# Performance work log

Hardware: AMD Instinct MI355X
Metric: run time of the kernel (lower is better)

Reference implementation:

```python
import jax, jax.numpy as jnp
import numpy as np
from jax import lax

B_, C_, H_, W_ = 2, 128, 64, 64
N_LAYERS = 2
D_STATE = 16
D_INNER = 2 * C_          # mamba expand=2
D_CONV = 4
DT_RANK = (C_ + 15) // 16  # ceil(d_model/16) = 8


def _layernorm(x, g, b, eps=1e-5):
    m = jnp.mean(x, axis=-1, keepdims=True)
    v = jnp.mean(jnp.square(x - m), axis=-1, keepdims=True)
    return (x - m) * lax.rsqrt(v + eps) * g + b


def _mamba(x, in_w, conv_w, conv_b, xproj_w, dt_w, dt_b, A_log, ssm_D, out_w):
    # x: (B, L, C)
    B, L, C = x.shape
    di, N = A_log.shape
    R = dt_w.shape[1]
    xz = x @ in_w.T                              # (B, L, 2*di)
    u, z = jnp.split(xz, 2, axis=-1)
    # causal depthwise conv1d, kernel d_conv, left-pad d_conv-1
    uc = u.transpose(0, 2, 1)                    # (B, di, L)
    uc = lax.conv_general_dilated(uc, conv_w, (1,), [(D_CONV - 1, 0)],
                                  feature_group_count=di)
    uc = uc + conv_b[None, :, None]
    u = jax.nn.silu(uc.transpose(0, 2, 1))       # (B, L, di)
    dbl = u @ xproj_w.T                          # (B, L, R+2N)
    dt, Bm, Cm = jnp.split(dbl, [R, R + N], axis=-1)
    dt = jax.nn.softplus(dt @ dt_w.T + dt_b)     # (B, L, di)
    A = -jnp.exp(A_log)                          # (di, N)
    dA = jnp.exp(dt[..., None] * A)              # (B, L, di, N)
    dBu = (dt * u)[..., None] * Bm[:, :, None, :]  # (B, L, di, N)

    def step(h, inp):
        dA_t, dBu_t, C_t = inp
        h = dA_t * h + dBu_t                     # (B, di, N)
        y = jnp.einsum('bdn,bn->bd', h, C_t)
        return h, y

    h0 = jnp.zeros((B, di, N), x.dtype)
    _, ys = lax.scan(step, h0, (dA.transpose(1, 0, 2, 3),
                                dBu.transpose(1, 0, 2, 3),
                                Cm.transpose(1, 0, 2)))
    y = ys.transpose(1, 0, 2) + u * ssm_D        # (B, L, di)
    y = y * jax.nn.silu(z)
    return y @ out_w.T                           # (B, L, C)


def setup_inputs() -> dict:
    key = jax.random.key(0)
    ks = jax.random.split(key, 24)
    C, di, N, R, L4 = C_, D_INNER, D_STATE, DT_RANK, 4 * C_
    s = lambda f: 1.0 / np.sqrt(f)
    inp = {
        'x': jax.random.normal(ks[0], (B_, C_, H_, W_), jnp.float32),
        'embed_w': jax.random.normal(ks[1], (C, C), jnp.float32) * s(C),
        'embed_b': jnp.zeros((C,), jnp.float32),
        'outc_w': jax.random.normal(ks[2], (C, C), jnp.float32) * s(C),
        'outc_b': jnp.zeros((C,), jnp.float32),
        'ln_g': jnp.ones((N_LAYERS, C), jnp.float32),
        'ln_b': jnp.zeros((N_LAYERS, C), jnp.float32),
        'in_w': jax.random.normal(ks[3], (N_LAYERS, 2 * di, C), jnp.float32) * s(C),
        'conv_w': jax.random.normal(ks[4], (N_LAYERS, di, 1, D_CONV), jnp.float32) * s(D_CONV),
        'conv_b': jnp.zeros((N_LAYERS, di), jnp.float32),
        'xproj_w': jax.random.normal(ks[5], (N_LAYERS, R + 2 * N, di), jnp.float32) * s(di),
        'dtproj_w': jax.random.normal(ks[6], (N_LAYERS, di, R), jnp.float32) * s(R),
        'dtproj_b': jax.random.uniform(ks[7], (N_LAYERS, di), jnp.float32, -4.0, -2.0),
        'A_log': jnp.tile(jnp.log(jnp.arange(1, N + 1, dtype=jnp.float32))[None, None, :],
                          (N_LAYERS, di, 1)),
        'ssm_D': jnp.ones((N_LAYERS, di), jnp.float32),
        'mout_w': jax.random.normal(ks[8], (N_LAYERS, C, di), jnp.float32) * s(di),
        'ffn_w1': jax.random.normal(ks[9], (N_LAYERS, L4, C), jnp.float32) * s(C),
        'ffn_b1': jnp.zeros((N_LAYERS, L4), jnp.float32),
        'ffn_w2': jax.random.normal(ks[10], (N_LAYERS, C, L4), jnp.float32) * s(L4),
        'ffn_b2': jnp.zeros((N_LAYERS, C), jnp.float32),
    }
    return inp


def reference(x, embed_w, embed_b, outc_w, outc_b, ln_g, ln_b, in_w, conv_w,
              conv_b, xproj_w, dtproj_w, dtproj_b, A_log, ssm_D, mout_w,
              ffn_w1, ffn_b1, ffn_w2, ffn_b2):
    B, C, H, W = x.shape
    residual = x
    h = jnp.einsum('bchw,oc->bohw', x, embed_w) + embed_b[None, :, None, None]
    t = h.reshape(B, C, H * W).transpose(0, 2, 1)   # (B, L, C)
    for i in range(N_LAYERS):
        r = t
        t2 = _layernorm(t, ln_g[i], ln_b[i])
        t2 = _mamba(t2, in_w[i], conv_w[i], conv_b[i], xproj_w[i],
                    dtproj_w[i], dtproj_b[i], A_log[i], ssm_D[i], mout_w[i])
        t = t2 + r
        r = t
        t2 = _layernorm(t, ln_g[i], ln_b[i])  # same LN params reused (as in source)
        t2 = jax.nn.gelu(t2 @ ffn_w1[i].T + ffn_b1[i], approximate=False)
        t2 = t2 @ ffn_w2[i].T + ffn_b2[i]
        t = t2 + r
    y = t.transpose(0, 2, 1).reshape(B, C, H, W)
    y = jnp.einsum('bchw,oc->bohw', y, outc_w) + outc_b[None, :, None, None]
    return residual + y
```

## Files before the change

kernel.cpp:

```cpp
#include <hip/hip_runtime.h>
#include <hip/hip_bf16.h>


#define LSEQ 4096
#define BLC  8192
#define NC   64
#define CHK  64
#define NCH  8192

typedef __attribute__((ext_vector_type(4))) float f32x4;
typedef __attribute__((ext_vector_type(8))) short s16x8;

__device__ __forceinline__ unsigned short f2bu(float f) {
    unsigned u = __float_as_uint(f);
    return (unsigned short)((u + 0x7fffu + ((u >> 16) & 1u)) >> 16);
}

template<bool ADD>
__global__ __launch_bounds__(256) void transpose_kernel(
    const float* __restrict__ in_, float* __restrict__ out_,
    const float* __restrict__ add, int R, int Cc)
{
    __shared__ float tile[32][33];
    size_t boff = (size_t)blockIdx.z * R * Cc;
    int r0 = blockIdx.y * 32, c0 = blockIdx.x * 32;
    int tx = threadIdx.x, ty = threadIdx.y;
#pragma unroll
    for (int j = 0; j < 4; ++j)
        tile[ty + j * 8][tx] = in_[boff + (size_t)(r0 + ty + j * 8) * Cc + (c0 + tx)];
    __syncthreads();
#pragma unroll
    for (int j = 0; j < 4; ++j) {
        size_t idx = boff + (size_t)(c0 + ty + j * 8) * R + (r0 + tx);
        float v = tile[tx][ty + j * 8];
        if (ADD) v += add[idx];
        out_[idx] = v;
    }
}

__global__ __launch_bounds__(256) void transposeDT(
    const float* __restrict__ dt, const float* __restrict__ u,
    float* __restrict__ dtT, float* __restrict__ dtuT)
{
    __shared__ float t1[32][33];
    __shared__ float t2[32][33];
    int r0 = blockIdx.y * 32, c0 = blockIdx.x * 32;
    int tx = threadIdx.x, ty = threadIdx.y;
#pragma unroll
    for (int j = 0; j < 4; ++j) {
        size_t idx = (size_t)(r0 + ty + j * 8) * 256 + (c0 + tx);
        float a = dt[idx], b = u[idx];
        t1[ty + j * 8][tx] = a;
        t2[ty + j * 8][tx] = a * b;
    }
    __syncthreads();
#pragma unroll
    for (int j = 0; j < 4; ++j) {
        size_t o = (size_t)(c0 + ty + j * 8) * BLC + (r0 + tx);
        dtT [o] = t1[tx][ty + j * 8];
        dtuT[o] = t2[tx][ty + j * 8];
    }
}

template<int BM, int ACT, bool BIAS, bool RES, bool SPLIT, bool EPI>
__global__ __launch_bounds__(256) void mgemm(
    const float* __restrict__ X, const float* __restrict__ W,
    const float* __restrict__ bias, const float* __restrict__ res,
    const float* __restrict__ pu, const float* __restrict__ pz,
    const float* __restrict__ pD,
    float* __restrict__ Y, float* __restrict__ Y2, int N, int K)
{
    constexpr int MF = BM / 32;
    __shared__ __align__(16) unsigned short Xs[BM * 64];
    __shared__ __align__(16) unsigned short Ws[64 * 64];
    int tid  = threadIdx.x;
    int lane = tid & 63;
    int wave = tid >> 6;
    int wm = wave >> 1, wn = wave & 1;
    int l15 = lane & 15, l4 = lane >> 4;
    int bm = blockIdx.x * BM, bn = blockIdx.y * 64;
    f32x4 acc[MF][2] = {};

    int q  = tid & 15;
    int r0 = tid >> 4;

    for (int k0 = 0; k0 < K; k0 += 64) {
        __syncthreads();
#pragma unroll
        for (int p = 0; p < BM / 16; ++p) {
            int row = r0 + p * 16;
            size_t gi = (size_t)(bm + row) * K + k0 + q * 4;
            float4 v = *(const float4*)&X[gi];
            if (EPI) {
                float4 u4 = *(const float4*)&pu[gi];
                float4 z4 = *(const float4*)&pz[gi];
                float4 D4 = *(const float4*)&pD[k0 + q * 4];
                v.x = fmaf(u4.x, D4.x, v.x) * (z4.x / (1.f + __expf(-z4.x)));
                v.y = fmaf(u4.y, D4.y, v.y) * (z4.y / (1.f + __expf(-z4.y)));
                v.z = fmaf(u4.z, D4.z, v.z) * (z4.z / (1.f + __expf(-z4.z)));
                v.w = fmaf(u4.w, D4.w, v.w) * (z4.w / (1.f + __expf(-z4.w)));
            }
            unsigned lo = f2bu(v.x) | ((unsigned)f2bu(v.y) << 16);
            unsigned hi = f2bu(v.z) | ((unsigned)f2bu(v.w) << 16);
            int off = (row * 128 + q * 8) ^ ((row & 7) << 4);
            *(uint2*)((char*)Xs + off) = make_uint2(lo, hi);
        }
#pragma unroll
        for (int p = 0; p < 4; ++p) {
            int row = r0 + p * 16;
            float4 v = *(const float4*)&W[(size_t)(bn + row) * K + k0 + q * 4];
            unsigned lo = f2bu(v.x) | ((unsigned)f2bu(v.y) << 16);
            unsigned hi = f2bu(v.z) | ((unsigned)f2bu(v.w) << 16);
            int off = (row * 128 + q * 8) ^ ((row & 7) << 4);
            *(uint2*)((char*)Ws + off) = make_uint2(lo, hi);
        }
        __syncthreads();
#pragma unroll
        for (int ks = 0; ks < 2; ++ks) {
            s16x8 a[MF], b[2];
#pragma unroll
            for (int mf = 0; mf < MF; ++mf) {
                int row = wm * (BM / 2) + mf * 16 + l15;
                int off = (row * 128 + (ks * 32 + l4 * 8) * 2) ^ ((row & 7) << 4);
                a[mf] = *(const s16x8*)((const char*)Xs + off);
            }
#pragma unroll
            for (int nf = 0; nf < 2; ++nf) {
                int row = wn * 32 + nf * 16 + l15;
                int off = (row * 128 + (ks * 32 + l4 * 8) * 2) ^ ((row & 7) << 4);
                b[nf] = *(const s16x8*)((const char*)Ws + off);
            }
#pragma unroll
            for (int mf = 0; mf < MF; ++mf)
#pragma unroll
                for (int nf = 0; nf < 2; ++nf)
                    acc[mf][nf] = __builtin_amdgcn_mfma_f32_16x16x32_bf16(
                        a[mf], b[nf], acc[mf][nf], 0, 0, 0);
        }
    }

#pragma unroll
    for (int mf = 0; mf < MF; ++mf) {
#pragma unroll
        for (int nf = 0; nf < 2; ++nf) {
            int col   = bn + wn * 32 + nf * 16 + l15;
            int rbase = bm + wm * (BM / 2) + mf * 16 + l4 * 4;
            float bv = BIAS ? bias[col] : 0.f;
#pragma unroll
            for (int r = 0; r < 4; ++r) {
                float v = acc[mf][nf][r] + bv;
                if (ACT == 2) v = 0.5f * v * (1.f + erff(v * 0.70710678118654752f));
                if (SPLIT) {
                    if (col < 256) Y [(size_t)(rbase + r) * 256 + col]       = v;
                    else           Y2[(size_t)(rbase + r) * 256 + col - 256] = v;
                } else {
                    size_t o = (size_t)(rbase + r) * N + col;
                    if (RES) v += res[o];
                    Y[o] = v;
                }
            }
        }
    }
}

template<int ACT, bool BIAS>
__global__ __launch_bounds__(256) void gemm_kernel(
    const float* __restrict__ X, int lda,
    const float* __restrict__ W,
    const float* __restrict__ bias,
    float* __restrict__ Y, int N, int K)
{
    __shared__ __align__(16) float As[16][68];
    __shared__ __align__(16) float Ws[16][68];
    int bm = blockIdx.x * 64;
    int bn = blockIdx.y * 64;
    int tid = threadIdx.x;
    int tm = (tid >> 4) << 2;
    int tn = (tid & 15) << 2;
    float acc[4][4] = {};

    for (int k0 = 0; k0 < K; k0 += 16) {
#pragma unroll
        for (int i = 0; i < 4; ++i) {
            int idx = tid + i * 256;
            int m  = idx >> 4;
            int kk = idx & 15;
            int gk = k0 + kk;
            As[kk][m] = (gk < K) ? X[(size_t)(bm + m) * lda + gk] : 0.f;
            int gn = bn + m;
            Ws[kk][m] = (gk < K && gn < N) ? W[(size_t)gn * K + gk] : 0.f;
        }
        __syncthreads();
#pragma unroll
        for (int kk = 0; kk < 16; ++kk) {
            float4 av = *reinterpret_cast<const float4*>(&As[kk][tm]);
            float4 bv = *reinterpret_cast<const float4*>(&Ws[kk][tn]);
            float a[4] = {av.x, av.y, av.z, av.w};
            float b[4] = {bv.x, bv.y, bv.z, bv.w};
#pragma unroll
            for (int i2 = 0; i2 < 4; ++i2)
#pragma unroll
                for (int j2 = 0; j2 < 4; ++j2)
                    acc[i2][j2] = fmaf(a[i2], b[j2], acc[i2][j2]);
        }
        __syncthreads();
    }
#pragma unroll
    for (int i2 = 0; i2 < 4; ++i2) {
        int gm = bm + tm + i2;
#pragma unroll
        for (int j2 = 0; j2 < 4; ++j2) {
            int gn = bn + tn + j2;
            if (gn < N) {
                float v = acc[i2][j2];
                if (BIAS) v += bias[gn];
                if (ACT == 1) v = (v > 0.f) ? v + log1pf(expf(-v)) : log1pf(expf(v));
                Y[(size_t)gm * N + gn] = v;
            }
        }
    }
}

__global__ __launch_bounds__(256) void ln_kernel(
    const float* __restrict__ X, const float* __restrict__ g,
    const float* __restrict__ bb, float* __restrict__ Y)
{
    int row  = blockIdx.x * 4 + (threadIdx.x >> 6);
    int lane = threadIdx.x & 63;
    const float* xr = X + (size_t)row * 128;
    float v0 = xr[lane], v1 = xr[lane + 64];
    float s = v0 + v1;
#pragma unroll
    for (int off = 32; off > 0; off >>= 1) s += __shfl_xor(s, off, 64);
    float mean = s * 0.0078125f;
    float d0 = v0 - mean, d1 = v1 - mean;
    float q = d0 * d0 + d1 * d1;
#pragma unroll
    for (int off = 32; off > 0; off >>= 1) q += __shfl_xor(q, off, 64);
    float rstd = rsqrtf(q * 0.0078125f + 1e-5f);
    float* yr = Y + (size_t)row * 128;
    yr[lane]      = d0 * rstd * g[lane]      + bb[lane];
    yr[lane + 64] = d1 * rstd * g[lane + 64] + bb[lane + 64];
}

__global__ __launch_bounds__(256) void conv_silu_kernel(
    const float* __restrict__ u, const float* __restrict__ cw,
    const float* __restrict__ cb, float* __restrict__ out)
{
    int i   = blockIdx.x * 256 + threadIdx.x;
    int dq  = (i & 63) << 2;
    int row = i >> 6;
    int l   = row & (LSEQ - 1);
    float4 a = *(const float4*)&cb[dq];
    float w[4][4];
#pragma unroll
    for (int e = 0; e < 4; ++e) {
        float4 we = *(const float4*)&cw[(dq + e) * 4];
        w[e][0] = we.x; w[e][1] = we.y; w[e][2] = we.z; w[e][3] = we.w;
    }
#pragma unroll
    for (int j = 0; j < 4; ++j) {
        if (l >= 3 - j) {
            const float4 v = *(const float4*)&u[(size_t)(row - 3 + j) * 256 + dq];
            a.x = fmaf(v.x, w[0][j], a.x);
            a.y = fmaf(v.y, w[1][j], a.y);
            a.z = fmaf(v.z, w[2][j], a.z);
            a.w = fmaf(v.w, w[3][j], a.w);
        }
    }
    float4 o;
    o.x = a.x / (1.f + __expf(-a.x));
    o.y = a.y / (1.f + __expf(-a.y));
    o.z = a.z / (1.f + __expf(-a.z));
    o.w = a.w / (1.f + __expf(-a.w));
    *(float4*)&out[(size_t)row * 256 + dq] = o;
}

__global__ __launch_bounds__(256) void scan_phase1(
    const float* __restrict__ dtT, const float* __restrict__ dtuT,
    const float* __restrict__ dbl, const float* __restrict__ A_log,
    float* __restrict__ hend, float* __restrict__ aprod)
{
    int g    = threadIdx.x & 3;
    int dloc = threadIdx.x >> 2;
    int d    = blockIdx.x * 64 + dloc;
    int c    = blockIdx.y;
    int b    = blockIdx.z;
    float4 al = *(const float4*)&A_log[d * 16 + g * 4];
    float A0 = -__expf(al.x), A1 = -__expf(al.y), A2 = -__expf(al.z), A3 = -__expf(al.w);
    int base = d * BLC + b * LSEQ + c * CHK;
    int row0 = b * LSEQ + c * CHK;
    float h0 = 0.f, h1 = 0.f, h2 = 0.f, h3 = 0.f;
    float p0 = 1.f, p1 = 1.f, p2 = 1.f, p3 = 1.f;
#pragma unroll 2
    for (int t4 = 0; t4 < CHK; t4 += 4) {
        float4 dt4 = *(const float4*)&dtT [base + t4];
        float4 du4 = *(const float4*)&dtuT[base + t4];
        float dts[4] = {dt4.x, dt4.y, dt4.z, dt4.w};
        float dus[4] = {du4.x, du4.y, du4.z, du4.w};
#pragma unroll
        for (int j = 0; j < 4; ++j) {
            float4 B4 = *(const float4*)&dbl[(size_t)(row0 + t4 + j) * 40 + 8 + g * 4];
            float a0 = __expf(dts[j] * A0), a1 = __expf(dts[j] * A1);
            float a2 = __expf(dts[j] * A2), a3 = __expf(dts[j] * A3);
            h0 = fmaf(a0, h0, dus[j] * B4.x); p0 *= a0;
            h1 = fmaf(a1, h1, dus[j] * B4.y); p1 *= a1;
            h2 = fmaf(a2, h2, dus[j] * B4.z); p2 *= a2;
            h3 = fmaf(a3, h3, dus[j] * B4.w); p3 *= a3;
        }
    }
    int ch = (b * 256 + d) * 16 + g * 4;
    *(float4*)&hend [c * NCH + ch] = make_float4(h0, h1, h2, h3);
    *(float4*)&aprod[c * NCH + ch] = make_float4(p0, p1, p2, p3);
}

__global__ __launch_bounds__(256) void scan_phase2(
    const float* __restrict__ hend, float* __restrict__ apr_h0)
{
    int ch = blockIdx.x * 256 + threadIdx.x;
    float h = 0.f;
#pragma unroll
    for (int c = 0; c < NC; ++c) {
        float ap = apr_h0[c * NCH + ch];
        float he = hend[c * NCH + ch];
        apr_h0[c * NCH + ch] = h;
        h = fmaf(ap, h, he);
    }
}

__global__ __launch_bounds__(256) void scan_phase3(
    const float* __restrict__ dtT, const float* __restrict__ dtuT,
    const float* __restrict__ dbl, const float* __restrict__ A_log,
    const float* __restrict__ h0b, float* __restrict__ y)
{
    int g    = threadIdx.x & 3;
    int dloc = threadIdx.x >> 2;
    int d    = blockIdx.x * 64 + dloc;
    int c    = blockIdx.y;
    int b    = blockIdx.z;
    float4 al = *(const float4*)&A_log[d * 16 + g * 4];
    float A0 = -__expf(al.x), A1 = -__expf(al.y), A2 = -__expf(al.z), A3 = -__expf(al.w);
    int base = d * BLC + b * LSEQ + c * CHK;
    int row0 = b * LSEQ + c * CHK;
    int ch = (b * 256 + d) * 16 + g * 4;
    float4 hv = *(const float4*)&h0b[c * NCH + ch];
    float h0 = hv.x, h1 = hv.y, h2 = hv.z, h3 = hv.w;
#pragma unroll 2
    for (int t4 = 0; t4 < CHK; t4 += 4) {
        float4 dt4 = *(const float4*)&dtT [base + t4];
        float4 du4 = *(const float4*)&dtuT[base + t4];
        float dts[4] = {dt4.x, dt4.y, dt4.z, dt4.w};
        float dus[4] = {du4.x, du4.y, du4.z, du4.w};
#pragma unroll
        for (int j = 0; j < 4; ++j) {
            size_t rb = (size_t)(row0 + t4 + j) * 40;
            float4 B4 = *(const float4*)&dbl[rb + 8  + g * 4];
            float4 C4 = *(const float4*)&dbl[rb + 24 + g * 4];
            float a0 = __expf(dts[j] * A0), a1 = __expf(dts[j] * A1);
            float a2 = __expf(dts[j] * A2), a3 = __expf(dts[j] * A3);
            h0 = fmaf(a0, h0, dus[j] * B4.x);
            h1 = fmaf(a1, h1, dus[j] * B4.y);
            h2 = fmaf(a2, h2, dus[j] * B4.z);
            h3 = fmaf(a3, h3, dus[j] * B4.w);
            float p = h0 * C4.x;
            p = fmaf(h1, C4.y, p);
            p = fmaf(h2, C4.z, p);
            p = fmaf(h3, C4.w, p);
            p += __shfl_xor(p, 1);
            p += __shfl_xor(p, 2);
            if (g == 0) y[(size_t)(row0 + t4 + j) * 256 + d] = p;
        }
    }
}

extern "C" void kernel_launch(void* const* d_in, const int* in_sizes, int n_in,
                              void* d_out, int out_size, void* d_ws, size_t ws_size,
                              hipStream_t stream)
{
    const float* x        = (const float*)d_in[0];
    const float* embed_w  = (const float*)d_in[1];
    const float* embed_b  = (const float*)d_in[2];
    const float* outc_w   = (const float*)d_in[3];
    const float* outc_b   = (const float*)d_in[4];
    const float* ln_g     = (const float*)d_in[5];
    const float* ln_b     = (const float*)d_in[6];
    const float* in_w     = (const float*)d_in[7];
    const float* conv_w   = (const float*)d_in[8];
    const float* conv_b   = (const float*)d_in[9];
    const float* xproj_w  = (const float*)d_in[10];
    const float* dtproj_w = (const float*)d_in[11];
    const float* dtproj_b = (const float*)d_in[12];
    const float* A_log    = (const float*)d_in[13];
    const float* ssm_D    = (const float*)d_in[14];
    const float* mout_w   = (const float*)d_in[15];
    const float* ffn_w1   = (const float*)d_in[16];
    const float* ffn_b1   = (const float*)d_in[17];
    const float* ffn_w2   = (const float*)d_in[18];
    const float* ffn_b2   = (const float*)d_in[19];

    float* ws   = (float*)d_ws;
    float* t    = ws;
    float* tmp2 = ws + 1048576;
    float* ub   = ws + 3145728;
    float* zb   = ws + 5242880;
    float* ucv  = ws + 7340032;
    float* dtb  = ws + 9437184;
    float* dbl  = ws + 11534336;
    float* hend = ws + 11862016;
    float* apr  = ws + 12386304;
    float* out  = (float*)d_out;

    float* dtT    = ub;
    float* dtuT   = tmp2;
    float* ffnmid = ub;

    dim3 tb(32, 8);
    transpose_kernel<false><<<dim3(128, 4, 2), tb, 0, stream>>>(x, tmp2, nullptr, 128, 4096);
    mgemm<64, 0, true, false, false, false><<<dim3(128, 2), 256, 0, stream>>>(
        tmp2, embed_w, embed_b, nullptr, nullptr, nullptr, nullptr, t, nullptr, 128, 128);

    for (int i = 0; i < 2; ++i) {
        ln_kernel<<<2048, 256, 0, stream>>>(t, ln_g + i * 128, ln_b + i * 128, tmp2);
        mgemm<128, 0, false, false, true, false><<<dim3(64, 8), 256, 0, stream>>>(
            tmp2, in_w + i * 65536, nullptr, nullptr, nullptr, nullptr, nullptr, ub, zb, 512, 128);
        conv_silu_kernel<<<2048, 256, 0, stream>>>(ub, conv_w + i * 1024, conv_b + i * 256, ucv);
        gemm_kernel<0, false><<<dim3(128, 1), 256, 0, stream>>>(ucv, 256, xproj_w + i * 10240, nullptr, dbl, 40, 256);
        gemm_kernel<1, true><<<dim3(128, 4), 256, 0, stream>>>(dbl, 40, dtproj_w + i * 2048, dtproj_b + i * 256, dtb, 256, 8);
        transposeDT<<<dim3(8, 256), tb, 0, stream>>>(dtb, ucv, dtT, dtuT);
        scan_phase1<<<dim3(4, NC, 2), 256, 0, stream>>>(dtT, dtuT, dbl, A_log + i * 4096, hend, apr);
        scan_phase2<<<32, 256, 0, stream>>>(hend, apr);
        scan_phase3<<<dim3(4, NC, 2), 256, 0, stream>>>(dtT, dtuT, dbl, A_log + i * 4096, apr, dtb);
        mgemm<64, 0, false, true, false, true><<<dim3(128, 2), 256, 0, stream>>>(
            dtb, mout_w + i * 32768, nullptr, t, ucv, zb, ssm_D + i * 256, t, nullptr, 128, 256);
        ln_kernel<<<2048, 256, 0, stream>>>(t, ln_g + i * 128, ln_b + i * 128, tmp2);
        mgemm<128, 2, true, false, false, false><<<dim3(64, 8), 256, 0, stream>>>(
            tmp2, ffn_w1 + i * 65536, ffn_b1 + i * 512, nullptr, nullptr, nullptr, nullptr, ffnmid, nullptr, 512, 128);
        mgemm<64, 0, true, true, false, false><<<dim3(128, 2), 256, 0, stream>>>(
            ffnmid, ffn_w2 + i * 65536, ffn_b2 + i * 128, t, nullptr, nullptr, nullptr, t, nullptr, 128, 512);
    }

    mgemm<64, 0, true, false, false, false><<<dim3(128, 2), 256, 0, stream>>>(
        t, outc_w, outc_b, nullptr, nullptr, nullptr, nullptr, tmp2, nullptr, 128, 128);
    transpose_kernel<true><<<dim3(4, 128, 2), tb, 0, stream>>>(tmp2, out, x, 4096, 128);
}
```

Before: 451.1 us.

## Fuse LayerNorm into GEMMs and merge x/dt projections into one MFMA GEMM

LayerNorm is folded into the prologue of the in-proj and FFN1 GEMMs, which normalize rows straight into bf16 shared memory and remove the separate LN kernels and their workspace round-trip. The x_proj and dt_proj weights are precombined into one 288x256 matrix, so a single bf16 MFMA GEMM produces dt, with softplus, dt*u and transposed outputs, plus B/C in a transposed layout. This replaces the two scalar fp32 GEMMs and the transpose kernel. The scan kernels now read B/C with coalesced float4 loads from that layout. The cost is that dt is computed through a pre-multiplied weight in bf16, which changes rounding, and in-proj/FFN1 blocks now do the LN work redundantly across their column tiles.

```diff
diff --git a/kernel.cpp b/kernel.cpp
--- a/kernel.cpp
+++ b/kernel.cpp
@@ -15,6 +15,9 @@
     unsigned u = __float_as_uint(f);
     return (unsigned short)((u + 0x7fffu + ((u >> 16) & 1u)) >> 16);
 }
+__device__ __forceinline__ float softplus_f(float v) {
+    return (v > 0.f) ? v + log1pf(expf(-v)) : log1pf(expf(v));
+}
 
 template<bool ADD>
 __global__ __launch_bounds__(256) void transpose_kernel(
@@ -38,37 +41,33 @@
     }
 }
 
-__global__ __launch_bounds__(256) void transposeDT(
-    const float* __restrict__ dt, const float* __restrict__ u,
-    float* __restrict__ dtT, float* __restrict__ dtuT)
-{
-    __shared__ float t1[32][33];
-    __shared__ float t2[32][33];
-    int r0 = blockIdx.y * 32, c0 = blockIdx.x * 32;
-    int tx = threadIdx.x, ty = threadIdx.y;
-#pragma unroll
-    for (int j = 0; j < 4; ++j) {
-        size_t idx = (size_t)(r0 + ty + j * 8) * 256 + (c0 + tx);
-        float a = dt[idx], b = u[idx];
-        t1[ty + j * 8][tx] = a;
-        t2[ty + j * 8][tx] = a * b;
-    }
-    __syncthreads();
-#pragma unroll
-    for (int j = 0; j < 4; ++j) {
-        size_t o = (size_t)(c0 + ty + j * 8) * BLC + (r0 + tx);
-        dtT [o] = t1[tx][ty + j * 8];
-        dtuT[o] = t2[tx][ty + j * 8];
-    }
-}
-
-template<int BM, int ACT, bool BIAS, bool RES, bool SPLIT, bool EPI>
+__global__ __launch_bounds__(256) void build_wcomb(
+    const float* __restrict__ xproj_w, const float* __restrict__ dtproj_w,
+    float* __restrict__ wc)
+{
+    int i = blockIdx.x * 256 + threadIdx.x;
+    int layer = i / 81920;
+    int rem   = i - layer * 81920;
+    int row = rem >> 8, col = rem & 255;
+    const float* xp = xproj_w + layer * 10240;
+    float v = 0.f;
+    if (row < 256) {
+        const float* dw = dtproj_w + layer * 2048 + row * 8;
+#pragma unroll
+        for (int r = 0; r < 8; ++r) v = fmaf(dw[r], xp[r * 256 + col], v);
+    } else if (row < 288) {
+        v = xp[(8 + row - 256) * 256 + col];
+    }
+    wc[i] = v;
+}
+
+template<int BM, int ACT, bool BIAS, bool RES, bool EPI>
 __global__ __launch_bounds__(256) void mgemm(
     const float* __restrict__ X, const float* __restrict__ W,
     const float* __restrict__ bias, const float* __restrict__ res,
     const float* __restrict__ pu, const float* __restrict__ pz,
     const float* __restrict__ pD,
-    float* __restrict__ Y, float* __restrict__ Y2, int N, int K)
+    float* __restrict__ Y, int N, int K)
 {
     constexpr int MF = BM / 32;
     __shared__ __align__(16) unsigned short Xs[BM * 64];
@@ -80,7 +79,6 @@
     int l15 = lane & 15, l4 = lane >> 4;
     int bm = blockIdx.x * BM, bn = blockIdx.y * 64;
     f32x4 acc[MF][2] = {};
-
     int q  = tid & 15;
     int r0 = tid >> 4;
 
@@ -150,97 +148,228 @@
             for (int r = 0; r < 4; ++r) {
                 float v = acc[mf][nf][r] + bv;
                 if (ACT == 2) v = 0.5f * v * (1.f + erff(v * 0.70710678118654752f));
+                size_t o = (size_t)(rbase + r) * N + col;
+                if (RES) v += res[o];
+                Y[o] = v;
+            }
+        }
+    }
+}
+
+template<int ACT, bool BIAS, bool SPLIT>
+__global__ __launch_bounds__(256) void mgemm_ln(
+    const float* __restrict__ X,
+    const float* __restrict__ lng, const float* __restrict__ lnb,
+    const float* __restrict__ W, const float* __restrict__ bias,
+    float* __restrict__ Y, float* __restrict__ Y2, int N)
+{
+    __shared__ __align__(16) unsigned short Xs[128 * 128];
+    __shared__ __align__(16) unsigned short Ws[64 * 64];
+    int tid  = threadIdx.x;
+    int lane = tid & 63;
+    int wave = tid >> 6;
+    int wm = wave >> 1, wn = wave & 1;
+    int l15 = lane & 15, l4 = lane >> 4;
+    int bm = blockIdx.x * 128, bn = blockIdx.y * 64;
+
+    int rsub = lane >> 4;
+    int cg   = lane & 15;
+    float4 ga = *(const float4*)&lng[cg * 8], gb = *(const float4*)&lng[cg * 8 + 4];
+    float4 ba = *(const float4*)&lnb[cg * 8], bb2 = *(const float4*)&lnb[cg * 8 + 4];
+#pragma unroll 2
+    for (int it = 0; it < 8; ++it) {
+        int row = wave * 32 + it * 4 + rsub;
+        const float* xr = X + (size_t)(bm + row) * 128 + cg * 8;
+        float4 xa = *(const float4*)xr;
+        float4 xb = *(const float4*)(xr + 4);
+        float s = xa.x + xa.y + xa.z + xa.w + xb.x + xb.y + xb.z + xb.w;
+        float q = xa.x*xa.x + xa.y*xa.y + xa.z*xa.z + xa.w*xa.w
+                + xb.x*xb.x + xb.y*xb.y + xb.z*xb.z + xb.w*xb.w;
+        s += __shfl_xor(s, 1, 16); q += __shfl_xor(q, 1, 16);
+        s += __shfl_xor(s, 2, 16); q += __shfl_xor(q, 2, 16);
+        s += __shfl_xor(s, 4, 16); q += __shfl_xor(q, 4, 16);
+        s += __shfl_xor(s, 8, 16); q += __shfl_xor(q, 8, 16);
+        float mean = s * 0.0078125f;
+        float var  = fmaf(-mean, mean, q * 0.0078125f);
+        float rstd = rsqrtf(var + 1e-5f);
+        float o0 = fmaf((xa.x - mean) * rstd, ga.x, ba.x);
+        float o1 = fmaf((xa.y - mean) * rstd, ga.y, ba.y);
+        float o2 = fmaf((xa.z - mean) * rstd, ga.z, ba.z);
+        float o3 = fmaf((xa.w - mean) * rstd, ga.w, ba.w);
+        float o4 = fmaf((xb.x - mean) * rstd, gb.x, bb2.x);
+        float o5 = fmaf((xb.y - mean) * rstd, gb.y, bb2.y);
+        float o6 = fmaf((xb.z - mean) * rstd, gb.z, bb2.z);
+        float o7 = fmaf((xb.w - mean) * rstd, gb.w, bb2.w);
+        uint4 wv;
+        wv.x = f2bu(o0) | ((unsigned)f2bu(o1) << 16);
+        wv.y = f2bu(o2) | ((unsigned)f2bu(o3) << 16);
+        wv.z = f2bu(o4) | ((unsigned)f2bu(o5) << 16);
+        wv.w = f2bu(o6) | ((unsigned)f2bu(o7) << 16);
+        int off = (row * 256 + cg * 16) ^ ((row & 7) << 4);
+        *(uint4*)((char*)Xs + off) = wv;
+    }
+
+    f32x4 acc[4][2] = {};
+    int q4 = tid & 15, r0 = tid >> 4;
+    for (int k0 = 0; k0 < 128; k0 += 64) {
+#pragma unroll
+        for (int p = 0; p < 4; ++p) {
+            int row = r0 + p * 16;
+            float4 v = *(const float4*)&W[(size_t)(bn + row) * 128 + k0 + q4 * 4];
+            unsigned lo = f2bu(v.x) | ((unsigned)f2bu(v.y) << 16);
+            unsigned hi = f2bu(v.z) | ((unsigned)f2bu(v.w) << 16);
+            int off = (row * 128 + q4 * 8) ^ ((row & 7) << 4);
+            *(uint2*)((char*)Ws + off) = make_uint2(lo, hi);
+        }
+        __syncthreads();
+#pragma unroll
+        for (int ks = 0; ks < 2; ++ks) {
+            s16x8 a[4], b[2];
+#pragma unroll
+            for (int mf = 0; mf < 4; ++mf) {
+                int row = wm * 64 + mf * 16 + l15;
+                int off = (row * 256 + (k0 + ks * 32 + l4 * 8) * 2) ^ ((row & 7) << 4);
+                a[mf] = *(const s16x8*)((const char*)Xs + off);
+            }
+#pragma unroll
+            for (int nf = 0; nf < 2; ++nf) {
+                int row = wn * 32 + nf * 16 + l15;
+                int off = (row * 128 + (ks * 32 + l4 * 8) * 2) ^ ((row & 7) << 4);
+                b[nf] = *(const s16x8*)((const char*)Ws + off);
+            }
+#pragma unroll
+            for (int mf = 0; mf < 4; ++mf)
+#pragma unroll
+                for (int nf = 0; nf < 2; ++nf)
+                    acc[mf][nf] = __builtin_amdgcn_mfma_f32_16x16x32_bf16(
+                        a[mf], b[nf], acc[mf][nf], 0, 0, 0);
+        }
+        __syncthreads();
+    }
+
+#pragma unroll
+    for (int mf = 0; mf < 4; ++mf) {
+#pragma unroll
+        for (int nf = 0; nf < 2; ++nf) {
+            int col   = bn + wn * 32 + nf * 16 + l15;
+            int rbase = bm + wm * 64 + mf * 16 + l4 * 4;
+            float bv = BIAS ? bias[col] : 0.f;
+#pragma unroll
+            for (int r = 0; r < 4; ++r) {
+                float v = acc[mf][nf][r] + bv;
+                if (ACT == 2) v = 0.5f * v * (1.f + erff(v * 0.70710678118654752f));
                 if (SPLIT) {
                     if (col < 256) Y [(size_t)(rbase + r) * 256 + col]       = v;
                     else           Y2[(size_t)(rbase + r) * 256 + col - 256] = v;
                 } else {
-                    size_t o = (size_t)(rbase + r) * N + col;
-                    if (RES) v += res[o];
-                    Y[o] = v;
+                    Y[(size_t)(rbase + r) * N + col] = v;
                 }
             }
         }
     }
 }
 
-template<int ACT, bool BIAS>
-__global__ __launch_bounds__(256) void gemm_kernel(
-    const float* __restrict__ X, int lda,
-    const float* __restrict__ W,
+__global__ __launch_bounds__(256) void mgemm_dtbc(
+    const float* __restrict__ Xu, const float* __restrict__ W,
     const float* __restrict__ bias,
-    float* __restrict__ Y, int N, int K)
-{
-    __shared__ __align__(16) float As[16][68];
-    __shared__ __align__(16) float Ws[16][68];
-    int bm = blockIdx.x * 64;
-    int bn = blockIdx.y * 64;
-    int tid = threadIdx.x;
-    int tm = (tid >> 4) << 2;
-    int tn = (tid & 15) << 2;
-    float acc[4][4] = {};
-
-    for (int k0 = 0; k0 < K; k0 += 16) {
-#pragma unroll
-        for (int i = 0; i < 4; ++i) {
-            int idx = tid + i * 256;
-            int m  = idx >> 4;
-            int kk = idx & 15;
-            int gk = k0 + kk;
-            As[kk][m] = (gk < K) ? X[(size_t)(bm + m) * lda + gk] : 0.f;
-            int gn = bn + m;
-            Ws[kk][m] = (gk < K && gn < N) ? W[(size_t)gn * K + gk] : 0.f;
-        }
+    float* __restrict__ dtT, float* __restrict__ dtuT, float* __restrict__ bct)
+{
+    __shared__ __align__(16) unsigned short Xs[128 * 64];
+    __shared__ __align__(16) unsigned short Ws[64 * 64];
+    int tid  = threadIdx.x;
+    int lane = tid & 63;
+    int wave = tid >> 6;
+    int wm = wave >> 1, wn = wave & 1;
+    int l15 = lane & 15, l4 = lane >> 4;
+    int bm = blockIdx.x * 128, bn = blockIdx.y * 64;
+    f32x4 acc[4][2] = {};
+    int q  = tid & 15;
+    int r0 = tid >> 4;
+
+    for (int k0 = 0; k0 < 256; k0 += 64) {
         __syncthreads();
 #pragma unroll
-        for (int kk = 0; kk < 16; ++kk) {
-            float4 av = *reinterpret_cast<const float4*>(&As[kk][tm]);
-            float4 bv = *reinterpret_cast<const float4*>(&Ws[kk][tn]);
-            float a[4] = {av.x, av.y, av.z, av.w};
-            float b[4] = {bv.x, bv.y, bv.z, bv.w};
-#pragma unroll
-            for (int i2 = 0; i2 < 4; ++i2)
-#pragma unroll
-                for (int j2 = 0; j2 < 4; ++j2)
-                    acc[i2][j2] = fmaf(a[i2], b[j2], acc[i2][j2]);
+        for (int p = 0; p < 8; ++p) {
+            int row = r0 + p * 16;
+            float4 v = *(const float4*)&Xu[(size_t)(bm + row) * 256 + k0 + q * 4];
+            unsigned lo = f2bu(v.x) | ((unsigned)f2bu(v.y) << 16);
+            unsigned hi = f2bu(v.z) | ((unsigned)f2bu(v.w) << 16);
+            int off = (row * 128 + q * 8) ^ ((row & 7) << 4);
+            *(uint2*)((char*)Xs + off) = make_uint2(lo, hi);
+        }
+#pragma unroll
+        for (int p = 0; p < 4; ++p) {
+            int row = r0 + p * 16;
+            float4 v = *(const float4*)&W[(size_t)(bn + row) * 256 + k0 + q * 4];
+            unsigned lo = f2bu(v.x) | ((unsigned)f2bu(v.y) << 16);
+            unsigned hi = f2bu(v.z) | ((unsigned)f2bu(v.w) << 16);
+            int off = (row * 128 + q * 8) ^ ((row & 7) << 4);
+            *(uint2*)((char*)Ws + off) = make_uint2(lo, hi);
         }
         __syncthreads();
-    }
-#pragma unroll
-    for (int i2 = 0; i2 < 4; ++i2) {
-        int gm = bm + tm + i2;
-#pragma unroll
-        for (int j2 = 0; j2 < 4; ++j2) {
-            int gn = bn + tn + j2;
-            if (gn < N) {
-                float v = acc[i2][j2];
-                if (BIAS) v += bias[gn];
-                if (ACT == 1) v = (v > 0.f) ? v + log1pf(expf(-v)) : log1pf(expf(v));
-                Y[(size_t)gm * N + gn] = v;
-            }
-        }
-    }
-}
-
-__global__ __launch_bounds__(256) void ln_kernel(
-    const float* __restrict__ X, const float* __restrict__ g,
-    const float* __restrict__ bb, float* __restrict__ Y)
-{
-    int row  = blockIdx.x * 4 + (threadIdx.x >> 6);
-    int lane = threadIdx.x & 63;
-    const float* xr = X + (size_t)row * 128;
-    float v0 = xr[lane], v1 = xr[lane + 64];
-    float s = v0 + v1;
-#pragma unroll
-    for (int off = 32; off > 0; off >>= 1) s += __shfl_xor(s, off, 64);
-    float mean = s * 0.0078125f;
-    float d0 = v0 - mean, d1 = v1 - mean;
-    float q = d0 * d0 + d1 * d1;
-#pragma unroll
-    for (int off = 32; off > 0; off >>= 1) q += __shfl_xor(q, off, 64);
-    float rstd = rsqrtf(q * 0.0078125f + 1e-5f);
-    float* yr = Y + (size_t)row * 128;
-    yr[lane]      = d0 * rstd * g[lane]      + bb[lane];
-    yr[lane + 64] = d1 * rstd * g[lane + 64] + bb[lane + 64];
+#pragma unroll
+        for (int ks = 0; ks < 2; ++ks) {
+            s16x8 a[4], b[2];
+#pragma unroll
+            for (int mf = 0; mf < 4; ++mf) {
+                int row = wm * 64 + mf * 16 + l15;
+                int off = (row * 128 + (ks * 32 + l4 * 8) * 2) ^ ((row & 7) << 4);
+                a[mf] = *(const s16x8*)((const char*)Xs + off);
+            }
+#pragma unroll
+            for (int nf = 0; nf < 2; ++nf) {
+                int row = wn * 32 + nf * 16 + l15;
+                int off = (row * 128 + (ks * 32 + l4 * 8) * 2) ^ ((row & 7) << 4);
+                b[nf] = *(const s16x8*)((const char*)Ws + off);
+            }
+#pragma unroll
+            for (int mf = 0; mf < 4; ++mf)
+#pragma unroll
+                for (int nf = 0; nf < 2; ++nf)
+                    acc[mf][nf] = __builtin_amdgcn_mfma_f32_16x16x32_bf16(
+                        a[mf], b[nf], acc[mf][nf], 0, 0, 0);
+        }
+    }
+
+    if (bn < 256) {
+#pragma unroll
+        for (int mf = 0; mf < 4; ++mf) {
+#pragma unroll
+            for (int nf = 0; nf < 2; ++nf) {
+                int col   = bn + wn * 32 + nf * 16 + l15;
+                int rbase = bm + wm * 64 + mf * 16 + l4 * 4;
+                float bv = bias[col];
+                float4 uu;
+                uu.x = Xu[(size_t)(rbase + 0) * 256 + col];
+                uu.y = Xu[(size_t)(rbase + 1) * 256 + col];
+                uu.z = Xu[(size_t)(rbase + 2) * 256 + col];
+                uu.w = Xu[(size_t)(rbase + 3) * 256 + col];
+                float4 dtv, duv;
+                float v0 = softplus_f(acc[mf][nf][0] + bv);
+                float v1 = softplus_f(acc[mf][nf][1] + bv);
+                float v2 = softplus_f(acc[mf][nf][2] + bv);
+                float v3 = softplus_f(acc[mf][nf][3] + bv);
+                dtv = make_float4(v0, v1, v2, v3);
+                duv = make_float4(v0 * uu.x, v1 * uu.y, v2 * uu.z, v3 * uu.w);
+                *(float4*)&dtT [(size_t)col * BLC + rbase] = dtv;
+                *(float4*)&dtuT[(size_t)col * BLC + rbase] = duv;
+            }
+        }
+    } else {
+#pragma unroll
+        for (int mf = 0; mf < 4; ++mf) {
+#pragma unroll
+            for (int nf = 0; nf < 2; ++nf) {
+                int col16 = wn * 32 + nf * 16 + l15;
+                int rbase = bm + wm * 64 + mf * 16 + l4 * 4;
+                if (col16 < 32) {
+                    float4 v = make_float4(acc[mf][nf][0], acc[mf][nf][1],
+                                           acc[mf][nf][2], acc[mf][nf][3]);
+                    *(float4*)&bct[(size_t)col16 * BLC + rbase] = v;
+                }
+            }
+        }
+    }
 }
 
 __global__ __launch_bounds__(256) void conv_silu_kernel(
@@ -278,7 +407,7 @@
 
 __global__ __launch_bounds__(256) void scan_phase1(
     const float* __restrict__ dtT, const float* __restrict__ dtuT,
-    const float* __restrict__ dbl, const float* __restrict__ A_log,
+    const float* __restrict__ bct, const float* __restrict__ A_log,
     float* __restrict__ hend, float* __restrict__ aprod)
 {
     int g    = threadIdx.x & 3;
@@ -288,25 +417,36 @@
     int b    = blockIdx.z;
     float4 al = *(const float4*)&A_log[d * 16 + g * 4];
     float A0 = -__expf(al.x), A1 = -__expf(al.y), A2 = -__expf(al.z), A3 = -__expf(al.w);
-    int base = d * BLC + b * LSEQ + c * CHK;
-    int row0 = b * LSEQ + c * CHK;
+    int base   = d * BLC + b * LSEQ + c * CHK;
+    int btbase = b * LSEQ + c * CHK;
+    const float* B0p = bct + (size_t)(g * 4 + 0) * BLC + btbase;
+    const float* B1p = B0p + BLC;
+    const float* B2p = B1p + BLC;
+    const float* B3p = B2p + BLC;
     float h0 = 0.f, h1 = 0.f, h2 = 0.f, h3 = 0.f;
     float p0 = 1.f, p1 = 1.f, p2 = 1.f, p3 = 1.f;
 #pragma unroll 2
     for (int t4 = 0; t4 < CHK; t4 += 4) {
         float4 dt4 = *(const float4*)&dtT [base + t4];
         float4 du4 = *(const float4*)&dtuT[base + t4];
+        float4 B0 = *(const float4*)(B0p + t4);
+        float4 B1 = *(const float4*)(B1p + t4);
+        float4 B2 = *(const float4*)(B2p + t4);
+        float4 B3 = *(const float4*)(B3p + t4);
         float dts[4] = {dt4.x, dt4.y, dt4.z, dt4.w};
         float dus[4] = {du4.x, du4.y, du4.z, du4.w};
+        float b0[4] = {B0.x, B0.y, B0.z, B0.w};
+        float b1[4] = {B1.x, B1.y, B1.z, B1.w};
+        float b2[4] = {B2.x, B2.y, B2.z, B2.w};
+        float b3[4] = {B3.x, B3.y, B3.z, B3.w};
 #pragma unroll
         for (int j = 0; j < 4; ++j) {
-            float4 B4 = *(const float4*)&dbl[(size_t)(row0 + t4 + j) * 40 + 8 + g * 4];
             float a0 = __expf(dts[j] * A0), a1 = __expf(dts[j] * A1);
             float a2 = __expf(dts[j] * A2), a3 = __expf(dts[j] * A3);
-            h0 = fmaf(a0, h0, dus[j] * B4.x); p0 *= a0;
-            h1 = fmaf(a1, h1, dus[j] * B4.y); p1 *= a1;
-            h2 = fmaf(a2, h2, dus[j] * B4.z); p2 *= a2;
-            h3 = fmaf(a3, h3, dus[j] * B4.w); p3 *= a3;
+            h0 = fmaf(a0, h0, dus[j] * b0[j]); p0 *= a0;
+            h1 = fmaf(a1, h1, dus[j] * b1[j]); p1 *= a1;
+            h2 = fmaf(a2, h2, dus[j] * b2[j]); p2 *= a2;
+            h3 = fmaf(a3, h3, dus[j] * b3[j]); p3 *= a3;
         }
     }
     int ch = (b * 256 + d) * 16 + g * 4;
@@ -330,7 +470,7 @@
 
 __global__ __launch_bounds__(256) void scan_phase3(
     const float* __restrict__ dtT, const float* __restrict__ dtuT,
-    const float* __restrict__ dbl, const float* __restrict__ A_log,
+    const float* __restrict__ bct, const float* __restrict__ A_log,
     const float* __restrict__ h0b, float* __restrict__ y)
 {
     int g    = threadIdx.x & 3;
@@ -340,8 +480,16 @@
     int b    = blockIdx.z;
     float4 al = *(const float4*)&A_log[d * 16 + g * 4];
     float A0 = -__expf(al.x), A1 = -__expf(al.y), A2 = -__expf(al.z), A3 = -__expf(al.w);
-    int base = d * BLC + b * LSEQ + c * CHK;
-    int row0 = b * LSEQ + c * CHK;
+    int base   = d * BLC + b * LSEQ + c * CHK;
+    int row0   = b * LSEQ + c * CHK;
+    const float* B0p = bct + (size_t)(g * 4 + 0) * BLC + row0;
+    const float* B1p = B0p + BLC;
+    const float* B2p = B1p + BLC;
+    const float* B3p = B2p + BLC;
+    const float* C0p = bct + (size_t)(16 + g * 4) * BLC + row0;
+    const float* C1p = C0p + BLC;
+    const float* C2p = C1p + BLC;
+    const float* C3p = C2p + BLC;
     int ch = (b * 256 + d) * 16 + g * 4;
     float4 hv = *(const float4*)&h0b[c * NCH + ch];
     float h0 = hv.x, h1 = hv.y, h2 = hv.z, h3 = hv.w;
@@ -349,23 +497,36 @@
     for (int t4 = 0; t4 < CHK; t4 += 4) {
         float4 dt4 = *(const float4*)&dtT [base + t4];
         float4 du4 = *(const float4*)&dtuT[base + t4];
+        float4 B0 = *(const float4*)(B0p + t4);
+        float4 B1 = *(const float4*)(B1p + t4);
+        float4 B2 = *(const float4*)(B2p + t4);
+        float4 B3 = *(const float4*)(B3p + t4);
+        float4 C0 = *(const float4*)(C0p + t4);
+        float4 C1 = *(const float4*)(C1p + t4);
+        float4 C2 = *(const float4*)(C2p + t4);
+        float4 C3 = *(const float4*)(C3p + t4);
         float dts[4] = {dt4.x, dt4.y, dt4.z, dt4.w};
         float dus[4] = {du4.x, du4.y, du4.z, du4.w};
+        float b0[4] = {B0.x, B0.y, B0.z, B0.w};
+        float b1[4] = {B1.x, B1.y, B1.z, B1.w};
+        float b2[4] = {B2.x, B2.y, B2.z, B2.w};
+        float b3[4] = {B3.x, B3.y, B3.z, B3.w};
+        float c0[4] = {C0.x, C0.y, C0.z, C0.w};
+        float c1[4] = {C1.x, C1.y, C1.z, C1.w};
+        float c2[4] = {C2.x, C2.y, C2.z, C2.w};
+        float c3[4] = {C3.x, C3.y, C3.z, C3.w};
 #pragma unroll
         for (int j = 0; j < 4; ++j) {
-            size_t rb = (size_t)(row0 + t4 + j) * 40;
-            float4 B4 = *(const float4*)&dbl[rb + 8  + g * 4];
-            float4 C4 = *(const float4*)&dbl[rb + 24 + g * 4];
             float a0 = __expf(dts[j] * A0), a1 = __expf(dts[j] * A1);
             float a2 = __expf(dts[j] * A2), a3 = __expf(dts[j] * A3);
-            h0 = fmaf(a0, h0, dus[j] * B4.x);
-            h1 = fmaf(a1, h1, dus[j] * B4.y);
-            h2 = fmaf(a2, h2, dus[j] * B4.z);
-            h3 = fmaf(a3, h3, dus[j] * B4.w);
-            float p = h0 * C4.x;
-            p = fmaf(h1, C4.y, p);
-            p = fmaf(h2, C4.z, p);
-            p = fmaf(h3, C4.w, p);
+            h0 = fmaf(a0, h0, dus[j] * b0[j]);
+            h1 = fmaf(a1, h1, dus[j] * b1[j]);
+            h2 = fmaf(a2, h2, dus[j] * b2[j]);
+            h3 = fmaf(a3, h3, dus[j] * b3[j]);
+            float p = h0 * c0[j];
+            p = fmaf(h1, c1[j], p);
+            p = fmaf(h2, c2[j], p);
+            p = fmaf(h3, c3[j], p);
             p += __shfl_xor(p, 1);
             p += __shfl_xor(p, 2);
             if (g == 0) y[(size_t)(row0 + t4 + j) * 256 + d] = p;
@@ -398,48 +559,47 @@
     const float* ffn_w2   = (const float*)d_in[18];
     const float* ffn_b2   = (const float*)d_in[19];
 
-    float* ws   = (float*)d_ws;
-    float* t    = ws;
-    float* tmp2 = ws + 1048576;
-    float* ub   = ws + 3145728;
-    float* zb   = ws + 5242880;
-    float* ucv  = ws + 7340032;
-    float* dtb  = ws + 9437184;
-    float* dbl  = ws + 11534336;
-    float* hend = ws + 11862016;
-    float* apr  = ws + 12386304;
-    float* out  = (float*)d_out;
+    float* ws    = (float*)d_ws;
+    float* t     = ws;
+    float* tmp2  = ws + 1048576;
+    float* ub    = ws + 3145728;
+    float* zb    = ws + 5242880;
+    float* ucv   = ws + 7340032;
+    float* dtb   = ws + 9437184;
+    float* bct   = ws + 11534336;
+    float* hend  = ws + 11796480;
+    float* apr   = ws + 12320768;
+    float* wcomb = ws + 12845056;
+    float* out   = (float*)d_out;
 
     float* dtT    = ub;
     float* dtuT   = tmp2;
     float* ffnmid = ub;
 
     dim3 tb(32, 8);
+    build_wcomb<<<640, 256, 0, stream>>>(xproj_w, dtproj_w, wcomb);
     transpose_kernel<false><<<dim3(128, 4, 2), tb, 0, stream>>>(x, tmp2, nullptr, 128, 4096);
-    mgemm<64, 0, true, false, false, false><<<dim3(128, 2), 256, 0, stream>>>(
-        tmp2, embed_w, embed_b, nullptr, nullptr, nullptr, nullptr, t, nullptr, 128, 128);
+    mgemm<64, 0, true, false, false><<<dim3(128, 2), 256, 0, stream>>>(
+        tmp2, embed_w, embed_b, nullptr, nullptr, nullptr, nullptr, t, 128, 128);
 
     for (int i = 0; i < 2; ++i) {
-        ln_kernel<<<2048, 256, 0, stream>>>(t, ln_g + i * 128, ln_b + i * 128, tmp2);
-        mgemm<128, 0, false, false, true, false><<<dim3(64, 8), 256, 0, stream>>>(
-            tmp2, in_w + i * 65536, nullptr, nullptr, nullptr, nullptr, nullptr, ub, zb, 512, 128);
+        mgemm_ln<0, false, true><<<dim3(64, 8), 256, 0, stream>>>(
+            t, ln_g + i * 128, ln_b + i * 128, in_w + i * 65536, nullptr, ub, zb, 512);
         conv_silu_kernel<<<2048, 256, 0, stream>>>(ub, conv_w + i * 1024, conv_b + i * 256, ucv);
-        gemm_kernel<0, false><<<dim3(128, 1), 256, 0, stream>>>(ucv, 256, xproj_w + i * 10240, nullptr, dbl, 40, 256);
-        gemm_kernel<1, true><<<dim3(128, 4), 256, 0, stream>>>(dbl, 40, dtproj_w + i * 2048, dtproj_b + i * 256, dtb, 256, 8);
-        transposeDT<<<dim3(8, 256), tb, 0, stream>>>(dtb, ucv, dtT, dtuT);
-        scan_phase1<<<dim3(4, NC, 2), 256, 0, stream>>>(dtT, dtuT, dbl, A_log + i * 4096, hend, apr);
+        mgemm_dtbc<<<dim3(64, 5), 256, 0, stream>>>(
+            ucv, wcomb + i * 81920, dtproj_b + i * 256, dtT, dtuT, bct);
+        scan_phase1<<<dim3(4, NC, 2), 256, 0, stream>>>(dtT, dtuT, bct, A_log + i * 4096, hend, apr);
         scan_phase2<<<32, 256, 0, stream>>>(hend, apr);
-        scan_phase3<<<dim3(4, NC, 2), 256, 0, stream>>>(dtT, dtuT, dbl, A_log + i * 4096, apr, dtb);
-        mgemm<64, 0, false, true, false, true><<<dim3(128, 2), 256, 0, stream>>>(
-            dtb, mout_w + i * 32768, nullptr, t, ucv, zb, ssm_D + i * 256, t, nullptr, 128, 256);
-        ln_kernel<<<2048, 256, 0, stream>>>(t, ln_g + i * 128, ln_b + i * 128, tmp2);
-        mgemm<128, 2, true, false, false, false><<<dim3(64, 8), 256, 0, stream>>>(
-            tmp2, ffn_w1 + i * 65536, ffn_b1 + i * 512, nullptr, nullptr, nullptr, nullptr, ffnmid, nullptr, 512, 128);
-        mgemm<64, 0, true, true, false, false><<<dim3(128, 2), 256, 0, stream>>>(
-            ffnmid, ffn_w2 + i * 65536, ffn_b2 + i * 128, t, nullptr, nullptr, nullptr, t, nullptr, 128, 512);
-    }
-
-    mgemm<64, 0, true, false, false, false><<<dim3(128, 2), 256, 0, stream>>>(
-        t, outc_w, outc_b, nullptr, nullptr, nullptr, nullptr, tmp2, nullptr, 128, 128);
+        scan_phase3<<<dim3(4, NC, 2), 256, 0, stream>>>(dtT, dtuT, bct, A_log + i * 4096, apr, dtb);
+        mgemm<64, 0, false, true, true><<<dim3(128, 2), 256, 0, stream>>>(
+            dtb, mout_w + i * 32768, nullptr, t, ucv, zb, ssm_D + i * 256, t, 128, 256);
+        mgemm_ln<2, true, false><<<dim3(64, 8), 256, 0, stream>>>(
+            t, ln_g + i * 128, ln_b + i * 128, ffn_w1 + i * 65536, ffn_b1 + i * 512, ffnmid, nullptr, 512);
+        mgemm<64, 0, true, true, false><<<dim3(128, 2), 256, 0, stream>>>(
+            ffnmid, ffn_w2 + i * 65536, ffn_b2 + i * 128, t, nullptr, nullptr, nullptr, t, 128, 512);
+    }
+
+    mgemm<64, 0, true, false, false><<<dim3(128, 2), 256, 0, stream>>>(
+        t, outc_w, outc_b, nullptr, nullptr, nullptr, nullptr, tmp2, 128, 128);
     transpose_kernel<true><<<dim3(4, 128, 2), tb, 0, stream>>>(tmp2, out, x, 4096, 128);
 }
```

Measured after the change: 427.4 us. 1.06x faster.
